# Optimization experiments

Hardware: AMD Instinct MI355X
Metric: run time of the kernel (lower is better)

## Reference

```python
import jax, jax.numpy as jnp
import numpy as np

N_NODES = 50000
N_EDGES = 800000
IN_DIM = 128
HID = 128
N_GRAPHS = 64


def setup_inputs() -> dict:
    key = jax.random.key(0)
    ks = jax.random.split(key, 12)
    edge_index = jax.random.randint(ks[0], (2, N_EDGES), 0, N_NODES, dtype=jnp.int64)
    edge_weight = jax.random.uniform(ks[1], (N_EDGES,), dtype=jnp.float32)
    input_feature = jax.random.normal(ks[2], (N_NODES, IN_DIM), dtype=jnp.float32)
    graph_indicator = jnp.sort(jax.random.randint(ks[3], (N_NODES,), 0, N_GRAPHS, dtype=jnp.int64))
    s = 0.05
    W1 = jax.random.normal(ks[4], (IN_DIM, HID), dtype=jnp.float32) * s
    b1 = jnp.zeros((HID,), jnp.float32)
    W2 = jax.random.normal(ks[5], (HID, HID), dtype=jnp.float32) * s
    b2 = jnp.zeros((HID,), jnp.float32)
    W3 = jax.random.normal(ks[6], (HID, HID), dtype=jnp.float32) * s
    b3 = jnp.zeros((HID,), jnp.float32)
    wa = jax.random.normal(ks[7], (3 * HID, 1), dtype=jnp.float32) * s
    ba = jnp.zeros((1,), jnp.float32)
    Wf = jax.random.normal(ks[8], (3 * HID * 2, IN_DIM), dtype=jnp.float32) * s
    bf = jnp.zeros((IN_DIM,), jnp.float32)
    return dict(edge_index=edge_index, edge_weight=edge_weight,
                input_feature=input_feature, graph_indicator=graph_indicator,
                W1=W1, b1=b1, W2=W2, b2=b2, W3=W3, b3=b3,
                wa=wa, ba=ba, Wf=Wf, bf=bf)


def reference(edge_index, edge_weight, input_feature, graph_indicator,
              W1, b1, W2, b2, W3, b3, wa, ba, Wf, bf):
    src, dst = edge_index[0], edge_index[1]

    def gcn(x, W, b):
        # GraphConvolution: adj @ (x @ W) + b, adj given as weighted edge list
        support = x @ W  # [N, d_out]
        msg = edge_weight[:, None] * support[src]  # [E, d_out] gather
        return jax.ops.segment_sum(msg, dst, num_segments=N_NODES) + b

    g1 = jax.nn.relu(gcn(input_feature, W1, b1))
    g2 = jax.nn.relu(gcn(g1, W2, b2))
    g3 = jax.nn.relu(gcn(g2, W3, b3))
    h = jnp.concatenate([g1, g2, g3], axis=1)  # [N, 3*HID]

    # SelfAttentionPooling: attention score via a 1-dim GraphConvolution, tanh gate
    score = jnp.tanh(gcn(h, wa, ba))  # [N, 1]
    pool = h * score

    # segment avg / max pooling per graph
    seg_sum = jax.ops.segment_sum(pool, graph_indicator, num_segments=N_GRAPHS)
    counts = jax.ops.segment_sum(jnp.ones((N_NODES, 1), pool.dtype), graph_indicator,
                                 num_segments=N_GRAPHS)
    avg = seg_sum / jnp.maximum(counts, 1.0)
    mx = jax.ops.segment_max(pool, graph_indicator, num_segments=N_GRAPHS)
    pooled = jnp.concatenate([avg, mx], axis=1)  # [G, 6*HID]

    return jax.nn.relu(pooled @ Wf + bf)  # [G, IN_DIM]
```

## Files before the change

kernel.cpp:

```cpp
#include <hip/hip_runtime.h>
#include <math.h>

#define HID 128
#define POOL_SEG 16
#define WT_STRIDE 136
#define ELL_D 48
#define SC_CHUNK 2048
#define FXS 16384.0f
#define FXI (1.0f/16384.0f)
#define FG_KC 12

typedef __attribute__((ext_vector_type(8))) short short8;
typedef __attribute__((ext_vector_type(4))) float float4v;

__device__ inline short f2bf(float f) {
  unsigned u = __builtin_bit_cast(unsigned, f);
  unsigned r = (u + 0x7fff + ((u >> 16) & 1)) >> 16;
  return (short)r;
}
__device__ inline unsigned pack2bf(float lo, float hi) {
  return (unsigned)(unsigned short)f2bf(lo) | ((unsigned)(unsigned short)f2bf(hi) << 16);
}
__device__ inline float bflo(unsigned u) { return __builtin_bit_cast(float, u << 16); }
__device__ inline float bfhi(unsigned u) { return __builtin_bit_cast(float, u & 0xffff0000u); }
__device__ inline float bf2f(unsigned short s) { return __builtin_bit_cast(float, (unsigned)s << 16); }
__device__ inline unsigned short f2h(float f) {
  _Float16 h = (_Float16)f;
  return __builtin_bit_cast(unsigned short, h);
}
__device__ inline float h2f(unsigned short hb) {
  return (float)__builtin_bit_cast(_Float16, hb);
}

__global__ void detect_flags(const int* __restrict__ ei, const int* __restrict__ gi,
                             int* __restrict__ flags, int n_nodes) {
  if (blockIdx.x == 0 && threadIdx.x == 0) {
    int nz = 0;
    for (int i = 1; i < 64; i += 2) nz |= ei[i];
    flags[0] = (nz == 0) ? 1 : 0;
    flags[1] = (gi[n_nodes - 1] == 0) ? 1 : 0;
  }
}

__global__ void prep_edges(const void* __restrict__ ei_raw, const int* __restrict__ flags,
                           const float* __restrict__ ew, int2* __restrict__ packed, int E) {
  int e = blockIdx.x * blockDim.x + threadIdx.x;
  if (e >= E) return;
  int s, d;
  if (flags[0]) {
    const long long* p = (const long long*)ei_raw;
    s = (int)p[e]; d = (int)p[E + e];
  } else {
    const int* p = (const int*)ei_raw;
    s = p[e]; d = p[E + e];
  }
  packed[e] = make_int2((d << 16) | s, __builtin_bit_cast(int, ew[e]));
}

__global__ void scatter_ell(const int2* __restrict__ packed, int* __restrict__ cursor,
                            unsigned* __restrict__ ell, int E, int N) {
  int group = blockIdx.x & 7;
  int chunk = blockIdx.x >> 3;
  int rng = (N + 7) >> 3;
  int lo = group * rng;
  int hi = lo + rng; if (hi > N) hi = N;
  int base = chunk * SC_CHUNK;
  for (int i = 0; i < SC_CHUNK; i += 256) {
    int e = base + i + threadIdx.x;
    if (e < E) {
      int2 rec = packed[e];
      int d = ((unsigned)rec.x) >> 16;
      if (d >= lo && d < hi) {
        unsigned s = (unsigned)rec.x & 0xFFFFu;
        unsigned short wh = f2h(__builtin_bit_cast(float, rec.y));
        int pos = atomicAdd(&cursor[d], 1);
        if (pos < ELL_D)
          ell[(size_t)d * ELL_D + pos] = (s << 16) | (unsigned)wh;
      }
    }
  }
}

__global__ void convert_w(const float* __restrict__ W1, const float* __restrict__ W2,
                          const float* __restrict__ W3, short* __restrict__ T1,
                          short* __restrict__ T2, short* __restrict__ T3) {
  int i = blockIdx.x * blockDim.x + threadIdx.x;
  int which = i >> 14, idx = i & 16383;
  int k = idx >> 7, n = idx & 127;
  const float* W = (which == 0) ? W1 : ((which == 1) ? W2 : W3);
  short* T = (which == 0) ? T1 : ((which == 1) ? T2 : T3);
  T[n * WT_STRIDE + k] = f2bf(W[idx]);
}

__global__ __launch_bounds__(256) void gemm_mfma(const float* __restrict__ Af,
                                                 const unsigned short* __restrict__ Abf,
                                                 const short* __restrict__ Wt,
                                                 unsigned short* __restrict__ C,
                                                 int n, int a_is_bf16) {
  __shared__ short Wlds[128 * WT_STRIDE];
  int t = threadIdx.x;
  {
    const ulonglong2* gsrc = (const ulonglong2*)Wt;
    ulonglong2* ldst = (ulonglong2*)Wlds;
    for (int i = t; i < (128 * WT_STRIDE) / 8; i += 256) ldst[i] = gsrc[i];
  }
  __syncthreads();

  int wave = t >> 6, lane = t & 63;
  int quad = lane >> 4, l15 = lane & 15;
  int m0 = blockIdx.x * 64 + wave * 16;

  int m = m0 + l15; if (m >= n) m = n - 1;
  short8 afrag[4];
  if (a_is_bf16) {
    const unsigned short* Arow = Abf + (size_t)m * 128;
#pragma unroll
    for (int c = 0; c < 4; c++) afrag[c] = *(const short8*)(Arow + c * 32 + quad * 8);
  } else {
    const float* Arow = Af + (size_t)m * 128;
#pragma unroll
    for (int c = 0; c < 4; c++) {
      int k0 = c * 32 + quad * 8;
      float4 x = *(const float4*)(Arow + k0);
      float4 y = *(const float4*)(Arow + k0 + 4);
      short8 a;
      a[0] = f2bf(x.x); a[1] = f2bf(x.y); a[2] = f2bf(x.z); a[3] = f2bf(x.w);
      a[4] = f2bf(y.x); a[5] = f2bf(y.y); a[6] = f2bf(y.z); a[7] = f2bf(y.w);
      afrag[c] = a;
    }
  }

  float4v acc[8];
#pragma unroll
  for (int tt = 0; tt < 8; tt++) acc[tt] = (float4v){0.f, 0.f, 0.f, 0.f};

#pragma unroll
  for (int c = 0; c < 4; c++) {
    int kb = c * 32 + quad * 8;
#pragma unroll
    for (int tt = 0; tt < 8; tt++) {
      const short8* bp = (const short8*)&Wlds[(tt * 16 + l15) * WT_STRIDE + kb];
      acc[tt] = __builtin_amdgcn_mfma_f32_16x16x32_bf16(afrag[c], *bp, acc[tt], 0, 0, 0);
    }
  }

  int rbase = m0 + quad * 4;
#pragma unroll
  for (int tt = 0; tt < 8; tt++) {
    int col = tt * 16 + l15;
#pragma unroll
    for (int r = 0; r < 4; r++) {
      int row = rbase + r;
      if (row < n) C[(size_t)row * 128 + col] = (unsigned short)f2bf(acc[tt][r]);
    }
  }
}

__global__ void aggregate(const unsigned short* __restrict__ support,
                          const int* __restrict__ deg_arr,
                          const unsigned* __restrict__ ell,
                          const float* __restrict__ bias, unsigned short* __restrict__ out,
                          const unsigned short* __restrict__ g1p,
                          const unsigned short* __restrict__ g2p,
                          const float* __restrict__ wa,
                          float* __restrict__ s_pre,
                          int n, int do_score) {
  int gid = blockIdx.x * blockDim.x + threadIdx.x;
  int node = gid >> 4, q = gid & 15;
  if (node >= n) return;
  int deg = deg_arr[node]; if (deg > ELL_D) deg = ELL_D;
  const unsigned* row = ell + (size_t)node * ELL_D;
  int acc[8];
#pragma unroll
  for (int j = 0; j < 8; j++) acc[j] = 0;
  const uint4* s4 = (const uint4*)support;

  int i = 0;
  for (; i + 3 < deg; i += 4) {
    unsigned r0 = row[i], r1 = row[i + 1], r2 = row[i + 2], r3 = row[i + 3];
    float w0 = h2f((unsigned short)(r0 & 0xFFFF)) * FXS;
    float w1 = h2f((unsigned short)(r1 & 0xFFFF)) * FXS;
    float w2 = h2f((unsigned short)(r2 & 0xFFFF)) * FXS;
    float w3 = h2f((unsigned short)(r3 & 0xFFFF)) * FXS;
    uint4 v0 = s4[(size_t)(r0 >> 16) * 16 + q];
    uint4 v1 = s4[(size_t)(r1 >> 16) * 16 + q];
    uint4 v2 = s4[(size_t)(r2 >> 16) * 16 + q];
    uint4 v3 = s4[(size_t)(r3 >> 16) * 16 + q];
    acc[0] += __float2int_rn(w0 * bflo(v0.x)); acc[1] += __float2int_rn(w0 * bfhi(v0.x));
    acc[2] += __float2int_rn(w0 * bflo(v0.y)); acc[3] += __float2int_rn(w0 * bfhi(v0.y));
    acc[4] += __float2int_rn(w0 * bflo(v0.z)); acc[5] += __float2int_rn(w0 * bfhi(v0.z));
    acc[6] += __float2int_rn(w0 * bflo(v0.w)); acc[7] += __float2int_rn(w0 * bfhi(v0.w));
    acc[0] += __float2int_rn(w1 * bflo(v1.x)); acc[1] += __float2int_rn(w1 * bfhi(v1.x));
    acc[2] += __float2int_rn(w1 * bflo(v1.y)); acc[3] += __float2int_rn(w1 * bfhi(v1.y));
    acc[4] += __float2int_rn(w1 * bflo(v1.z)); acc[5] += __float2int_rn(w1 * bfhi(v1.z));
    acc[6] += __float2int_rn(w1 * bflo(v1.w)); acc[7] += __float2int_rn(w1 * bfhi(v1.w));
    acc[0] += __float2int_rn(w2 * bflo(v2.x)); acc[1] += __float2int_rn(w2 * bfhi(v2.x));
    acc[2] += __float2int_rn(w2 * bflo(v2.y)); acc[3] += __float2int_rn(w2 * bfhi(v2.y));
    acc[4] += __float2int_rn(w2 * bflo(v2.z)); acc[5] += __float2int_rn(w2 * bfhi(v2.z));
    acc[6] += __float2int_rn(w2 * bflo(v2.w)); acc[7] += __float2int_rn(w2 * bfhi(v2.w));
    acc[0] += __float2int_rn(w3 * bflo(v3.x)); acc[1] += __float2int_rn(w3 * bfhi(v3.x));
    acc[2] += __float2int_rn(w3 * bflo(v3.y)); acc[3] += __float2int_rn(w3 * bfhi(v3.y));
    acc[4] += __float2int_rn(w3 * bflo(v3.z)); acc[5] += __float2int_rn(w3 * bfhi(v3.z));
    acc[6] += __float2int_rn(w3 * bflo(v3.w)); acc[7] += __float2int_rn(w3 * bfhi(v3.w));
  }
  for (; i < deg; i++) {
    unsigned r0 = row[i];
    float w0 = h2f((unsigned short)(r0 & 0xFFFF)) * FXS;
    uint4 v0 = s4[(size_t)(r0 >> 16) * 16 + q];
    acc[0] += __float2int_rn(w0 * bflo(v0.x)); acc[1] += __float2int_rn(w0 * bfhi(v0.x));
    acc[2] += __float2int_rn(w0 * bflo(v0.y)); acc[3] += __float2int_rn(w0 * bfhi(v0.y));
    acc[4] += __float2int_rn(w0 * bflo(v0.z)); acc[5] += __float2int_rn(w0 * bfhi(v0.z));
    acc[6] += __float2int_rn(w0 * bflo(v0.w)); acc[7] += __float2int_rn(w0 * bfhi(v0.w));
  }

  float f[8];
#pragma unroll
  for (int j = 0; j < 8; j++) f[j] = (float)acc[j] * FXI;

  float4 b0 = ((const float4*)bias)[q * 2];
  float4 b1 = ((const float4*)bias)[q * 2 + 1];
  f[0] = fmaxf(f[0] + b0.x, 0.f); f[1] = fmaxf(f[1] + b0.y, 0.f);
  f[2] = fmaxf(f[2] + b0.z, 0.f); f[3] = fmaxf(f[3] + b0.w, 0.f);
  f[4] = fmaxf(f[4] + b1.x, 0.f); f[5] = fmaxf(f[5] + b1.y, 0.f);
  f[6] = fmaxf(f[6] + b1.z, 0.f); f[7] = fmaxf(f[7] + b1.w, 0.f);

  uint4 o;
  o.x = pack2bf(f[0], f[1]); o.y = pack2bf(f[2], f[3]);
  o.z = pack2bf(f[4], f[5]); o.w = pack2bf(f[6], f[7]);
  ((uint4*)out)[(size_t)node * 16 + q] = o;

  if (do_score) {
    int d0 = q * 8;
    uint4 u1 = ((const uint4*)g1p)[(size_t)node * 16 + q];
    uint4 u2 = ((const uint4*)g2p)[(size_t)node * 16 + q];
    const float* wa1 = wa + d0;
    const float* wa2 = wa + 128 + d0;
    const float* wa3 = wa + 256 + d0;
    float sc = bflo(u1.x) * wa1[0] + bfhi(u1.x) * wa1[1]
             + bflo(u1.y) * wa1[2] + bfhi(u1.y) * wa1[3]
             + bflo(u1.z) * wa1[4] + bfhi(u1.z) * wa1[5]
             + bflo(u1.w) * wa1[6] + bfhi(u1.w) * wa1[7]
             + bflo(u2.x) * wa2[0] + bfhi(u2.x) * wa2[1]
             + bflo(u2.y) * wa2[2] + bfhi(u2.y) * wa2[3]
             + bflo(u2.z) * wa2[4] + bfhi(u2.z) * wa2[5]
             + bflo(u2.w) * wa2[6] + bfhi(u2.w) * wa2[7];
#pragma unroll
    for (int j = 0; j < 8; j++) sc += f[j] * wa3[j];
#pragma unroll
    for (int m = 1; m < 16; m <<= 1) sc += __shfl_xor(sc, m, 64);
    if (q == 0) s_pre[node] = sc;
  }
}

__global__ void att_aggregate(const float* __restrict__ s_pre, const int* __restrict__ deg_arr,
                              const unsigned* __restrict__ ell,
                              const float* __restrict__ ba, float* __restrict__ score, int n) {
  int node = blockIdx.x * blockDim.x + threadIdx.x;
  if (node >= n) return;
  int deg = deg_arr[node]; if (deg > ELL_D) deg = ELL_D;
  const unsigned* row = ell + (size_t)node * ELL_D;
  int acc = 0;
  for (int i = 0; i < deg; i++) {
    unsigned r = row[i];
    acc += __float2int_rn(h2f((unsigned short)(r & 0xFFFF)) * FXS * s_pre[r >> 16]);
  }
  score[node] = tanhf((float)acc * FXI + ba[0]);
}

__global__ void graph_bounds(const void* __restrict__ gi_raw, const int* __restrict__ flags,
                             int* __restrict__ gstart, int n, int ngraphs) {
  int g = threadIdx.x;
  if (g > ngraphs) return;
  if (g == ngraphs) { gstart[g] = n; return; }
  bool is64 = flags[1] != 0;
  const long long* g64 = (const long long*)gi_raw;
  const int* g32 = (const int*)gi_raw;
  int lo = 0, hi = n;
  while (lo < hi) {
    int mid = (lo + hi) >> 1;
    long long v = is64 ? g64[mid] : (long long)g32[mid];
    if (v < (long long)g) lo = mid + 1; else hi = mid;
  }
  gstart[g] = lo;
}

__global__ __launch_bounds__(384) void pool_partial(const unsigned short* __restrict__ g1,
                                                    const unsigned short* __restrict__ g2,
                                                    const unsigned short* __restrict__ g3,
                                                    const float* __restrict__ score,
                                                    const int* __restrict__ gstart,
                                                    float* __restrict__ part) {
  int g = blockIdx.x / POOL_SEG, seg = blockIdx.x % POOL_SEG;
  int d = threadIdx.x;
  int sg = d >> 7, dd = d & 127;
  const unsigned short* gp = (sg == 0) ? g1 : ((sg == 1) ? g2 : g3);
  int s = gstart[g], e = gstart[g + 1];
  int len = e - s;
  int chunk = (len + POOL_SEG - 1) / POOL_SEG;
  int ns = s + seg * chunk;
  int ne = ns + chunk; if (ne > e) ne = e;
  float sum = 0.f, mx = -3.402823466e38f;
  for (int node = ns; node < ne; node++) {
    float sc = score[node];
    float v = bf2f(gp[(size_t)node * 128 + dd]) * sc;
    sum += v;
    mx = fmaxf(mx, v);
  }
  size_t base = (size_t)blockIdx.x * 768;
  part[base + d] = sum;
  part[base + 384 + d] = mx;
}

__global__ __launch_bounds__(384) void pool_combine(const float* __restrict__ part,
                                                    const int* __restrict__ gstart,
                                                    float* __restrict__ pooled) {
  int g = blockIdx.x;
  int d = threadIdx.x;
  float sum = 0.f, mx = -3.402823466e38f;
  for (int seg = 0; seg < POOL_SEG; seg++) {
    size_t base = ((size_t)g * POOL_SEG + seg) * 768;
    sum += part[base + d];
    mx = fmaxf(mx, part[base + 384 + d]);
  }
  float cnt = (float)(gstart[g + 1] - gstart[g]);
  pooled[(size_t)g * 768 + d] = sum / fmaxf(cnt, 1.0f);
  pooled[(size_t)g * 768 + 384 + d] = mx;
}

__global__ __launch_bounds__(128) void fg_partial(const float* __restrict__ pooled,
                                                  const float* __restrict__ Wf,
                                                  float* __restrict__ fgp) {
  int g = blockIdx.x / FG_KC, kc = blockIdx.x % FG_KC;
  int c = threadIdx.x;
  __shared__ float row[64];
  if (c < 64) row[c] = pooled[(size_t)g * 768 + kc * 64 + c];
  __syncthreads();
  const float* Wp = Wf + (size_t)kc * 64 * 128 + c;
  float acc = 0.f;
#pragma unroll 8
  for (int k = 0; k < 64; k++) acc += row[k] * Wp[k * 128];
  fgp[((size_t)g * FG_KC + kc) * 128 + c] = acc;
}

__global__ __launch_bounds__(128) void fg_combine(const float* __restrict__ fgp,
                                                  const float* __restrict__ bf,
                                                  float* __restrict__ out) {
  int g = blockIdx.x;
  int c = threadIdx.x;
  float acc = bf[c];
#pragma unroll
  for (int kc = 0; kc < FG_KC; kc++)
    acc += fgp[((size_t)g * FG_KC + kc) * 128 + c];
  out[(size_t)g * 128 + c] = fmaxf(acc, 0.f);
}

extern "C" void kernel_launch(void* const* d_in, const int* in_sizes, int n_in,
                              void* d_out, int out_size, void* d_ws, size_t ws_size,
                              hipStream_t stream) {
  const void* ei_raw = d_in[0];
  const float* ew    = (const float*)d_in[1];
  const float* X     = (const float*)d_in[2];
  const void* gi_raw = d_in[3];
  const float* W1 = (const float*)d_in[4];  const float* b1 = (const float*)d_in[5];
  const float* W2 = (const float*)d_in[6];  const float* b2 = (const float*)d_in[7];
  const float* W3 = (const float*)d_in[8];  const float* b3 = (const float*)d_in[9];
  const float* wa = (const float*)d_in[10]; const float* ba = (const float*)d_in[11];
  const float* Wf = (const float*)d_in[12]; const float* bf = (const float*)d_in[13];
  float* out = (float*)d_out;

  const int E = in_sizes[1];
  const int N = in_sizes[2] / 128;
  const int G = out_size / 128;

  char* ws = (char*)d_ws;
  size_t off = 0;
  auto take = [&](size_t bytes) {
    char* p = ws + off;
    off = (off + bytes + 255) & ~(size_t)255;
    return p;
  };
  int*      flags   = (int*)take(16);
  int*      cursor  = (int*)take((size_t)N * 4);
  int2*     packed  = (int2*)take((size_t)E * 8);
  unsigned* ell     = (unsigned*)take((size_t)N * ELL_D * 4);
  short*    wt1     = (short*)take((size_t)128 * WT_STRIDE * 2);
  short*    wt2     = (short*)take((size_t)128 * WT_STRIDE * 2);
  short*    wt3     = (short*)take((size_t)128 * WT_STRIDE * 2);
  unsigned short* support = (unsigned short*)take((size_t)N * 128 * 2);
  unsigned short* g1      = (unsigned short*)take((size_t)N * 128 * 2);
  unsigned short* g2      = (unsigned short*)take((size_t)N * 128 * 2);
  unsigned short* g3      = (unsigned short*)take((size_t)N * 128 * 2);
  float* s_pre   = (float*)take((size_t)N * 4);
  float* score   = (float*)take((size_t)N * 4);
  int*   gstart  = (int*)take((size_t)(G + 1) * 4);
  float* part    = (float*)take((size_t)G * POOL_SEG * 768 * 4);
  float* pooled  = (float*)take((size_t)G * 768 * 4);
  float* fgp     = (float*)take((size_t)G * FG_KC * 128 * 4);
  if (off > ws_size) return;

  hipMemsetAsync(cursor, 0, (size_t)N * 4, stream);
  detect_flags<<<1, 64, 0, stream>>>((const int*)ei_raw, (const int*)gi_raw, flags, N);
  prep_edges<<<(E + 255) / 256, 256, 0, stream>>>(ei_raw, flags, ew, packed, E);
  convert_w<<<(3 * 16384 + 255) / 256, 256, 0, stream>>>(W1, W2, W3, wt1, wt2, wt3);
  {
    int chunks = (E + SC_CHUNK - 1) / SC_CHUNK;
    scatter_ell<<<8 * chunks, 256, 0, stream>>>(packed, cursor, ell, E, N);
  }

  const int GB = (N + 63) / 64;
  const int AB = (N * 16 + 255) / 256;
  gemm_mfma<<<GB, 256, 0, stream>>>(X, (const unsigned short*)nullptr, wt1, support, N, 0);
  aggregate<<<AB, 256, 0, stream>>>(support, cursor, ell, b1, g1,
                                    nullptr, nullptr, nullptr, nullptr, N, 0);
  gemm_mfma<<<GB, 256, 0, stream>>>((const float*)nullptr, g1, wt2, support, N, 1);
  aggregate<<<AB, 256, 0, stream>>>(support, cursor, ell, b2, g2,
                                    nullptr, nullptr, nullptr, nullptr, N, 0);
  gemm_mfma<<<GB, 256, 0, stream>>>((const float*)nullptr, g2, wt3, support, N, 1);
  aggregate<<<AB, 256, 0, stream>>>(support, cursor, ell, b3, g3,
                                    g1, g2, wa, s_pre, N, 1);

  att_aggregate<<<(N + 255) / 256, 256, 0, stream>>>(s_pre, cursor, ell, ba, score, N);

  graph_bounds<<<1, 128, 0, stream>>>(gi_raw, flags, gstart, N, G);
  pool_partial<<<G * POOL_SEG, 384, 0, stream>>>(g1, g2, g3, score, gstart, part);
  pool_combine<<<G, 384, 0, stream>>>(part, gstart, pooled);
  fg_partial<<<G * FG_KC, 128, 0, stream>>>(pooled, Wf, fgp);
  fg_combine<<<G, 128, 0, stream>>>(fgp, bf, out);
}
```

Before: 325.5 us.

## Slice feature layout into 32-column planes and fuse prologue and tail kernels

```diff
diff --git a/kernel.cpp b/kernel.cpp
--- a/kernel.cpp
+++ b/kernel.cpp
@@ -8,7 +8,6 @@
 #define SC_CHUNK 2048
 #define FXS 16384.0f
 #define FXI (1.0f/16384.0f)
-#define FG_KC 12
 
 typedef __attribute__((ext_vector_type(8))) short short8;
 typedef __attribute__((ext_vector_type(4))) float float4v;
@@ -32,29 +31,54 @@
   return (float)__builtin_bit_cast(_Float16, hb);
 }
 
-__global__ void detect_flags(const int* __restrict__ ei, const int* __restrict__ gi,
-                             int* __restrict__ flags, int n_nodes) {
-  if (blockIdx.x == 0 && threadIdx.x == 0) {
-    int nz = 0;
-    for (int i = 1; i < 64; i += 2) nz |= ei[i];
-    flags[0] = (nz == 0) ? 1 : 0;
-    flags[1] = (gi[n_nodes - 1] == 0) ? 1 : 0;
-  }
-}
-
-__global__ void prep_edges(const void* __restrict__ ei_raw, const int* __restrict__ flags,
-                           const float* __restrict__ ew, int2* __restrict__ packed, int E) {
-  int e = blockIdx.x * blockDim.x + threadIdx.x;
-  if (e >= E) return;
-  int s, d;
-  if (flags[0]) {
-    const long long* p = (const long long*)ei_raw;
-    s = (int)p[e]; d = (int)p[E + e];
+__global__ __launch_bounds__(256) void prologue(
+    const void* __restrict__ ei_raw, const float* __restrict__ ew,
+    int2* __restrict__ packed, int* __restrict__ cursor, int* __restrict__ s_pre_fx,
+    const float* __restrict__ W1, const float* __restrict__ W2, const float* __restrict__ W3,
+    short* __restrict__ T1, short* __restrict__ T2, short* __restrict__ T3,
+    const void* __restrict__ gi_raw, int* __restrict__ gstart,
+    int E, int N, int G, int EB) {
+  int b = blockIdx.x, t = threadIdx.x;
+  if (b < EB) {
+    int gid = b * 256 + t;
+    if (gid < N) { cursor[gid] = 0; s_pre_fx[gid] = 0; }
+    if (gid < E) {
+      const int* pw = (const int*)ei_raw;
+      int nz = 0;
+#pragma unroll
+      for (int i = 1; i < 64; i += 2) nz |= pw[i];
+      int s, d;
+      if (nz == 0) {
+        const long long* p = (const long long*)ei_raw;
+        s = (int)p[gid]; d = (int)p[E + gid];
+      } else {
+        const int* p = (const int*)ei_raw;
+        s = p[gid]; d = p[E + gid];
+      }
+      packed[gid] = make_int2((d << 16) | s, __builtin_bit_cast(int, ew[gid]));
+    }
+  } else if (b < EB + 192) {
+    int i = (b - EB) * 256 + t;
+    int which = i >> 14, idx = i & 16383;
+    int k = idx >> 7, nn = idx & 127;
+    const float* W = (which == 0) ? W1 : ((which == 1) ? W2 : W3);
+    short* T = (which == 0) ? T1 : ((which == 1) ? T2 : T3);
+    T[nn * WT_STRIDE + k] = f2bf(W[idx]);
   } else {
-    const int* p = (const int*)ei_raw;
-    s = p[e]; d = p[E + e];
-  }
-  packed[e] = make_int2((d << 16) | s, __builtin_bit_cast(int, ew[e]));
+    int g = t;
+    if (g > G) return;
+    if (g == G) { gstart[g] = N; return; }
+    bool is64 = (((const int*)gi_raw)[N - 1] == 0);
+    const long long* g64 = (const long long*)gi_raw;
+    const int* g32 = (const int*)gi_raw;
+    int lo = 0, hi = N;
+    while (lo < hi) {
+      int mid = (lo + hi) >> 1;
+      long long v = is64 ? g64[mid] : (long long)g32[mid];
+      if (v < (long long)g) lo = mid + 1; else hi = mid;
+    }
+    gstart[g] = lo;
+  }
 }
 
 __global__ void scatter_ell(const int2* __restrict__ packed, int* __restrict__ cursor,
@@ -81,17 +105,6 @@
   }
 }
 
-__global__ void convert_w(const float* __restrict__ W1, const float* __restrict__ W2,
-                          const float* __restrict__ W3, short* __restrict__ T1,
-                          short* __restrict__ T2, short* __restrict__ T3) {
-  int i = blockIdx.x * blockDim.x + threadIdx.x;
-  int which = i >> 14, idx = i & 16383;
-  int k = idx >> 7, n = idx & 127;
-  const float* W = (which == 0) ? W1 : ((which == 1) ? W2 : W3);
-  short* T = (which == 0) ? T1 : ((which == 1) ? T2 : T3);
-  T[n * WT_STRIDE + k] = f2bf(W[idx]);
-}
-
 __global__ __launch_bounds__(256) void gemm_mfma(const float* __restrict__ Af,
                                                  const unsigned short* __restrict__ Abf,
                                                  const short* __restrict__ Wt,
@@ -109,13 +122,14 @@
   int wave = t >> 6, lane = t & 63;
   int quad = lane >> 4, l15 = lane & 15;
   int m0 = blockIdx.x * 64 + wave * 16;
+  size_t SL = (size_t)n * 32;
 
   int m = m0 + l15; if (m >= n) m = n - 1;
   short8 afrag[4];
   if (a_is_bf16) {
-    const unsigned short* Arow = Abf + (size_t)m * 128;
-#pragma unroll
-    for (int c = 0; c < 4; c++) afrag[c] = *(const short8*)(Arow + c * 32 + quad * 8);
+#pragma unroll
+    for (int c = 0; c < 4; c++)
+      afrag[c] = *(const short8*)(Abf + c * SL + (size_t)m * 32 + quad * 8);
   } else {
     const float* Arow = Af + (size_t)m * 128;
 #pragma unroll
@@ -147,45 +161,52 @@
   int rbase = m0 + quad * 4;
 #pragma unroll
   for (int tt = 0; tt < 8; tt++) {
-    int col = tt * 16 + l15;
+    int within = (tt & 1) * 16 + l15;
+    size_t sb = (size_t)(tt >> 1) * SL;
 #pragma unroll
     for (int r = 0; r < 4; r++) {
       int row = rbase + r;
-      if (row < n) C[(size_t)row * 128 + col] = (unsigned short)f2bf(acc[tt][r]);
-    }
-  }
-}
-
-__global__ void aggregate(const unsigned short* __restrict__ support,
-                          const int* __restrict__ deg_arr,
-                          const unsigned* __restrict__ ell,
-                          const float* __restrict__ bias, unsigned short* __restrict__ out,
-                          const unsigned short* __restrict__ g1p,
-                          const unsigned short* __restrict__ g2p,
-                          const float* __restrict__ wa,
-                          float* __restrict__ s_pre,
-                          int n, int do_score) {
-  int gid = blockIdx.x * blockDim.x + threadIdx.x;
-  int node = gid >> 4, q = gid & 15;
+      if (row < n) C[sb + (size_t)row * 32 + within] = (unsigned short)f2bf(acc[tt][r]);
+    }
+  }
+}
+
+__global__ __launch_bounds__(256) void aggregate_sl(
+    const unsigned short* __restrict__ support, const int* __restrict__ deg_arr,
+    const unsigned* __restrict__ ell, const float* __restrict__ bias,
+    unsigned short* __restrict__ out,
+    const unsigned short* __restrict__ g1p, const unsigned short* __restrict__ g2p,
+    const float* __restrict__ wa, int* __restrict__ s_pre_fx,
+    int n, int halfN, int do_score) {
+  int g = blockIdx.x & 7;
+  int chunk = blockIdx.x >> 3;
+  int slice = g >> 1, half = g & 1;
+  int t = threadIdx.x;
+  int local = chunk * 64 + (t >> 2);
+  int q = t & 3;
+  if (local >= halfN) return;
+  int node = half * halfN + local;
   if (node >= n) return;
+
   int deg = deg_arr[node]; if (deg > ELL_D) deg = ELL_D;
   const unsigned* row = ell + (size_t)node * ELL_D;
+  const uint4* sb = (const uint4*)support + (size_t)slice * n * 4 + q;
+
   int acc[8];
 #pragma unroll
   for (int j = 0; j < 8; j++) acc[j] = 0;
-  const uint4* s4 = (const uint4*)support;
 
   int i = 0;
   for (; i + 3 < deg; i += 4) {
-    unsigned r0 = row[i], r1 = row[i + 1], r2 = row[i + 2], r3 = row[i + 3];
-    float w0 = h2f((unsigned short)(r0 & 0xFFFF)) * FXS;
-    float w1 = h2f((unsigned short)(r1 & 0xFFFF)) * FXS;
-    float w2 = h2f((unsigned short)(r2 & 0xFFFF)) * FXS;
-    float w3 = h2f((unsigned short)(r3 & 0xFFFF)) * FXS;
-    uint4 v0 = s4[(size_t)(r0 >> 16) * 16 + q];
-    uint4 v1 = s4[(size_t)(r1 >> 16) * 16 + q];
-    uint4 v2 = s4[(size_t)(r2 >> 16) * 16 + q];
-    uint4 v3 = s4[(size_t)(r3 >> 16) * 16 + q];
+    uint4 rr = *(const uint4*)(row + i);
+    float w0 = h2f((unsigned short)(rr.x & 0xFFFF)) * FXS;
+    float w1 = h2f((unsigned short)(rr.y & 0xFFFF)) * FXS;
+    float w2 = h2f((unsigned short)(rr.z & 0xFFFF)) * FXS;
+    float w3 = h2f((unsigned short)(rr.w & 0xFFFF)) * FXS;
+    uint4 v0 = sb[(size_t)(rr.x >> 16) * 4];
+    uint4 v1 = sb[(size_t)(rr.y >> 16) * 4];
+    uint4 v2 = sb[(size_t)(rr.z >> 16) * 4];
+    uint4 v3 = sb[(size_t)(rr.w >> 16) * 4];
     acc[0] += __float2int_rn(w0 * bflo(v0.x)); acc[1] += __float2int_rn(w0 * bfhi(v0.x));
     acc[2] += __float2int_rn(w0 * bflo(v0.y)); acc[3] += __float2int_rn(w0 * bfhi(v0.y));
     acc[4] += __float2int_rn(w0 * bflo(v0.z)); acc[5] += __float2int_rn(w0 * bfhi(v0.z));
@@ -206,7 +227,7 @@
   for (; i < deg; i++) {
     unsigned r0 = row[i];
     float w0 = h2f((unsigned short)(r0 & 0xFFFF)) * FXS;
-    uint4 v0 = s4[(size_t)(r0 >> 16) * 16 + q];
+    uint4 v0 = sb[(size_t)(r0 >> 16) * 4];
     acc[0] += __float2int_rn(w0 * bflo(v0.x)); acc[1] += __float2int_rn(w0 * bfhi(v0.x));
     acc[2] += __float2int_rn(w0 * bflo(v0.y)); acc[3] += __float2int_rn(w0 * bfhi(v0.y));
     acc[4] += __float2int_rn(w0 * bflo(v0.z)); acc[5] += __float2int_rn(w0 * bfhi(v0.z));
@@ -217,8 +238,8 @@
 #pragma unroll
   for (int j = 0; j < 8; j++) f[j] = (float)acc[j] * FXI;
 
-  float4 b0 = ((const float4*)bias)[q * 2];
-  float4 b1 = ((const float4*)bias)[q * 2 + 1];
+  float4 b0 = ((const float4*)bias)[slice * 8 + q * 2];
+  float4 b1 = ((const float4*)bias)[slice * 8 + q * 2 + 1];
   f[0] = fmaxf(f[0] + b0.x, 0.f); f[1] = fmaxf(f[1] + b0.y, 0.f);
   f[2] = fmaxf(f[2] + b0.z, 0.f); f[3] = fmaxf(f[3] + b0.w, 0.f);
   f[4] = fmaxf(f[4] + b1.x, 0.f); f[5] = fmaxf(f[5] + b1.y, 0.f);
@@ -227,15 +248,14 @@
   uint4 o;
   o.x = pack2bf(f[0], f[1]); o.y = pack2bf(f[2], f[3]);
   o.z = pack2bf(f[4], f[5]); o.w = pack2bf(f[6], f[7]);
-  ((uint4*)out)[(size_t)node * 16 + q] = o;
+  ((uint4*)out)[(size_t)slice * n * 4 + (size_t)node * 4 + q] = o;
 
   if (do_score) {
-    int d0 = q * 8;
-    uint4 u1 = ((const uint4*)g1p)[(size_t)node * 16 + q];
-    uint4 u2 = ((const uint4*)g2p)[(size_t)node * 16 + q];
-    const float* wa1 = wa + d0;
-    const float* wa2 = wa + 128 + d0;
-    const float* wa3 = wa + 256 + d0;
+    uint4 u1 = ((const uint4*)g1p)[(size_t)slice * n * 4 + (size_t)node * 4 + q];
+    uint4 u2 = ((const uint4*)g2p)[(size_t)slice * n * 4 + (size_t)node * 4 + q];
+    const float* wa1 = wa + slice * 32 + q * 8;
+    const float* wa2 = wa1 + 128;
+    const float* wa3 = wa1 + 256;
     float sc = bflo(u1.x) * wa1[0] + bfhi(u1.x) * wa1[1]
              + bflo(u1.y) * wa1[2] + bfhi(u1.y) * wa1[3]
              + bflo(u1.z) * wa1[4] + bfhi(u1.z) * wa1[5]
@@ -246,13 +266,13 @@
              + bflo(u2.w) * wa2[6] + bfhi(u2.w) * wa2[7];
 #pragma unroll
     for (int j = 0; j < 8; j++) sc += f[j] * wa3[j];
-#pragma unroll
-    for (int m = 1; m < 16; m <<= 1) sc += __shfl_xor(sc, m, 64);
-    if (q == 0) s_pre[node] = sc;
-  }
-}
-
-__global__ void att_aggregate(const float* __restrict__ s_pre, const int* __restrict__ deg_arr,
+    sc += __shfl_xor(sc, 1, 64);
+    sc += __shfl_xor(sc, 2, 64);
+    if (q == 0) atomicAdd(&s_pre_fx[node], __float2int_rn(sc * FXS));
+  }
+}
+
+__global__ void att_aggregate(const int* __restrict__ s_pre_fx, const int* __restrict__ deg_arr,
                               const unsigned* __restrict__ ell,
                               const float* __restrict__ ba, float* __restrict__ score, int n) {
   int node = blockIdx.x * blockDim.x + threadIdx.x;
@@ -262,26 +282,9 @@
   int acc = 0;
   for (int i = 0; i < deg; i++) {
     unsigned r = row[i];
-    acc += __float2int_rn(h2f((unsigned short)(r & 0xFFFF)) * FXS * s_pre[r >> 16]);
+    acc += __float2int_rn(h2f((unsigned short)(r & 0xFFFF)) * (float)s_pre_fx[r >> 16]);
   }
   score[node] = tanhf((float)acc * FXI + ba[0]);
-}
-
-__global__ void graph_bounds(const void* __restrict__ gi_raw, const int* __restrict__ flags,
-                             int* __restrict__ gstart, int n, int ngraphs) {
-  int g = threadIdx.x;
-  if (g > ngraphs) return;
-  if (g == ngraphs) { gstart[g] = n; return; }
-  bool is64 = flags[1] != 0;
-  const long long* g64 = (const long long*)gi_raw;
-  const int* g32 = (const int*)gi_raw;
-  int lo = 0, hi = n;
-  while (lo < hi) {
-    int mid = (lo + hi) >> 1;
-    long long v = is64 ? g64[mid] : (long long)g32[mid];
-    if (v < (long long)g) lo = mid + 1; else hi = mid;
-  }
-  gstart[g] = lo;
 }
 
 __global__ __launch_bounds__(384) void pool_partial(const unsigned short* __restrict__ g1,
@@ -289,11 +292,12 @@
                                                     const unsigned short* __restrict__ g3,
                                                     const float* __restrict__ score,
                                                     const int* __restrict__ gstart,
-                                                    float* __restrict__ part) {
+                                                    float* __restrict__ part, int n) {
   int g = blockIdx.x / POOL_SEG, seg = blockIdx.x % POOL_SEG;
   int d = threadIdx.x;
   int sg = d >> 7, dd = d & 127;
   const unsigned short* gp = (sg == 0) ? g1 : ((sg == 1) ? g2 : g3);
+  const unsigned short* col = gp + (size_t)(dd >> 5) * ((size_t)n * 32) + (dd & 31);
   int s = gstart[g], e = gstart[g + 1];
   int len = e - s;
   int chunk = (len + POOL_SEG - 1) / POOL_SEG;
@@ -302,7 +306,7 @@
   float sum = 0.f, mx = -3.402823466e38f;
   for (int node = ns; node < ne; node++) {
     float sc = score[node];
-    float v = bf2f(gp[(size_t)node * 128 + dd]) * sc;
+    float v = bf2f(col[(size_t)node * 32]) * sc;
     sum += v;
     mx = fmaxf(mx, v);
   }
@@ -311,47 +315,30 @@
   part[base + 384 + d] = mx;
 }
 
-__global__ __launch_bounds__(384) void pool_combine(const float* __restrict__ part,
-                                                    const int* __restrict__ gstart,
-                                                    float* __restrict__ pooled) {
-  int g = blockIdx.x;
-  int d = threadIdx.x;
-  float sum = 0.f, mx = -3.402823466e38f;
-  for (int seg = 0; seg < POOL_SEG; seg++) {
-    size_t base = ((size_t)g * POOL_SEG + seg) * 768;
-    sum += part[base + d];
-    mx = fmaxf(mx, part[base + 384 + d]);
-  }
+__global__ __launch_bounds__(128) void tail(const float* __restrict__ part,
+                                            const int* __restrict__ gstart,
+                                            const float* __restrict__ Wf,
+                                            const float* __restrict__ bfb,
+                                            float* __restrict__ out) {
+  __shared__ float pooled[768];
+  int g = blockIdx.x, t = threadIdx.x;
   float cnt = (float)(gstart[g + 1] - gstart[g]);
-  pooled[(size_t)g * 768 + d] = sum / fmaxf(cnt, 1.0f);
-  pooled[(size_t)g * 768 + 384 + d] = mx;
-}
-
-__global__ __launch_bounds__(128) void fg_partial(const float* __restrict__ pooled,
-                                                  const float* __restrict__ Wf,
-                                                  float* __restrict__ fgp) {
-  int g = blockIdx.x / FG_KC, kc = blockIdx.x % FG_KC;
-  int c = threadIdx.x;
-  __shared__ float row[64];
-  if (c < 64) row[c] = pooled[(size_t)g * 768 + kc * 64 + c];
+  float inv = 1.0f / fmaxf(cnt, 1.0f);
+  for (int d = t; d < 384; d += 128) {
+    float sum = 0.f, mx = -3.402823466e38f;
+    for (int seg = 0; seg < POOL_SEG; seg++) {
+      size_t base = ((size_t)g * POOL_SEG + seg) * 768;
+      sum += part[base + d];
+      mx = fmaxf(mx, part[base + 384 + d]);
+    }
+    pooled[d] = sum * inv;
+    pooled[384 + d] = mx;
+  }
   __syncthreads();
-  const float* Wp = Wf + (size_t)kc * 64 * 128 + c;
-  float acc = 0.f;
+  float acc = bfb[t];
 #pragma unroll 8
-  for (int k = 0; k < 64; k++) acc += row[k] * Wp[k * 128];
-  fgp[((size_t)g * FG_KC + kc) * 128 + c] = acc;
-}
-
-__global__ __launch_bounds__(128) void fg_combine(const float* __restrict__ fgp,
-                                                  const float* __restrict__ bf,
-                                                  float* __restrict__ out) {
-  int g = blockIdx.x;
-  int c = threadIdx.x;
-  float acc = bf[c];
-#pragma unroll
-  for (int kc = 0; kc < FG_KC; kc++)
-    acc += fgp[((size_t)g * FG_KC + kc) * 128 + c];
-  out[(size_t)g * 128 + c] = fmaxf(acc, 0.f);
+  for (int k = 0; k < 768; k++) acc += pooled[k] * Wf[(size_t)k * 128 + t];
+  out[(size_t)g * 128 + t] = fmaxf(acc, 0.f);
 }
 
 extern "C" void kernel_launch(void* const* d_in, const int* in_sizes, int n_in,
@@ -379,7 +366,6 @@
     off = (off + bytes + 255) & ~(size_t)255;
     return p;
   };
-  int*      flags   = (int*)take(16);
   int*      cursor  = (int*)take((size_t)N * 4);
   int2*     packed  = (int2*)take((size_t)E * 8);
   unsigned* ell     = (unsigned*)take((size_t)N * ELL_D * 4);
@@ -390,40 +376,36 @@
   unsigned short* g1      = (unsigned short*)take((size_t)N * 128 * 2);
   unsigned short* g2      = (unsigned short*)take((size_t)N * 128 * 2);
   unsigned short* g3      = (unsigned short*)take((size_t)N * 128 * 2);
-  float* s_pre   = (float*)take((size_t)N * 4);
-  float* score   = (float*)take((size_t)N * 4);
-  int*   gstart  = (int*)take((size_t)(G + 1) * 4);
-  float* part    = (float*)take((size_t)G * POOL_SEG * 768 * 4);
-  float* pooled  = (float*)take((size_t)G * 768 * 4);
-  float* fgp     = (float*)take((size_t)G * FG_KC * 128 * 4);
+  int*   s_pre_fx = (int*)take((size_t)N * 4);
+  float* score    = (float*)take((size_t)N * 4);
+  int*   gstart   = (int*)take((size_t)(G + 1) * 4);
+  float* part     = (float*)take((size_t)G * POOL_SEG * 768 * 4);
   if (off > ws_size) return;
 
-  hipMemsetAsync(cursor, 0, (size_t)N * 4, stream);
-  detect_flags<<<1, 64, 0, stream>>>((const int*)ei_raw, (const int*)gi_raw, flags, N);
-  prep_edges<<<(E + 255) / 256, 256, 0, stream>>>(ei_raw, flags, ew, packed, E);
-  convert_w<<<(3 * 16384 + 255) / 256, 256, 0, stream>>>(W1, W2, W3, wt1, wt2, wt3);
+  const int EB = (E + 255) / 256;
+  prologue<<<EB + 192 + 1, 256, 0, stream>>>(ei_raw, ew, packed, cursor, s_pre_fx,
+                                             W1, W2, W3, wt1, wt2, wt3,
+                                             gi_raw, gstart, E, N, G, EB);
   {
     int chunks = (E + SC_CHUNK - 1) / SC_CHUNK;
     scatter_ell<<<8 * chunks, 256, 0, stream>>>(packed, cursor, ell, E, N);
   }
 
   const int GB = (N + 63) / 64;
-  const int AB = (N * 16 + 255) / 256;
+  const int halfN = (N + 1) / 2;
+  const int AGB = 8 * ((halfN + 63) / 64);
   gemm_mfma<<<GB, 256, 0, stream>>>(X, (const unsigned short*)nullptr, wt1, support, N, 0);
-  aggregate<<<AB, 256, 0, stream>>>(support, cursor, ell, b1, g1,
-                                    nullptr, nullptr, nullptr, nullptr, N, 0);
+  aggregate_sl<<<AGB, 256, 0, stream>>>(support, cursor, ell, b1, g1,
+                                        nullptr, nullptr, nullptr, nullptr, N, halfN, 0);
   gemm_mfma<<<GB, 256, 0, stream>>>((const float*)nullptr, g1, wt2, support, N, 1);
-  aggregate<<<AB, 256, 0, stream>>>(support, cursor, ell, b2, g2,
-                                    nullptr, nullptr, nullptr, nullptr, N, 0);
+  aggregate_sl<<<AGB, 256, 0, stream>>>(support, cursor, ell, b2, g2,
+                                        nullptr, nullptr, nullptr, nullptr, N, halfN, 0);
   gemm_mfma<<<GB, 256, 0, stream>>>((const float*)nullptr, g2, wt3, support, N, 1);
-  aggregate<<<AB, 256, 0, stream>>>(support, cursor, ell, b3, g3,
-                                    g1, g2, wa, s_pre, N, 1);
-
-  att_aggregate<<<(N + 255) / 256, 256, 0, stream>>>(s_pre, cursor, ell, ba, score, N);
-
-  graph_bounds<<<1, 128, 0, stream>>>(gi_raw, flags, gstart, N, G);
-  pool_partial<<<G * POOL_SEG, 384, 0, stream>>>(g1, g2, g3, score, gstart, part);
-  pool_combine<<<G, 384, 0, stream>>>(part, gstart, pooled);
-  fg_partial<<<G * FG_KC, 128, 0, stream>>>(pooled, Wf, fgp);
-  fg_combine<<<G, 128, 0, stream>>>(fgp, bf, out);
-}
+  aggregate_sl<<<AGB, 256, 0, stream>>>(support, cursor, ell, b3, g3,
+                                        g1, g2, wa, s_pre_fx, N, halfN, 1);
+
+  att_aggregate<<<(N + 255) / 256, 256, 0, stream>>>(s_pre_fx, cursor, ell, ba, score, N);
+
+  pool_partial<<<G * POOL_SEG, 384, 0, stream>>>(g1, g2, g3, score, gstart, part, N);
+  tail<<<G, 128, 0, stream>>>(part, gstart, Wf, bf, out);
+}
```

New measurement: 344.8 us. 1.06x slower.
